# Performance work log

Hardware: AMD Instinct MI355X
Metric: run time of the kernel (lower is better)

The kernel has to match this reference:

```python
import jax, jax.numpy as jnp
import numpy as np

V, H, P, L, O = 47, 1024, 4, 3, 47
B, T = 256, 128


def setup_inputs() -> dict:
    key = jax.random.key(0)
    ks = jax.random.split(key, 10)
    s = 1.0 / np.sqrt(H)
    b_ih = jnp.zeros((L, 4 * H), jnp.float32).at[:, H:2 * H].set(1.0)  # forget-gate bias = 1
    return {
        "x": jax.random.randint(ks[0], (B, T), 0, V),
        "properties": jax.random.normal(ks[1], (B, P), jnp.float32),
        "emb": jax.random.normal(ks[2], (V, H), jnp.float32) * s,
        "W_dec": jax.random.normal(ks[3], (O, H), jnp.float32) * s,
        "b_dec": jnp.zeros((O,), jnp.float32),
        "W_ih0": jax.random.normal(ks[4], (4 * H, H + P), jnp.float32) * s,
        "W_ih_rest": jax.random.normal(ks[5], (L - 1, 4 * H, H), jnp.float32) * s,
        "W_hh": jax.random.normal(ks[6], (L, 4 * H, H), jnp.float32) * s,
        "b_ih": b_ih,
        "b_hh": jnp.zeros((L, 4 * H), jnp.float32),
    }


def _lstm_step(x_in, h, c, W_ih, W_hh, b_ih, b_hh):
    # x_in: [B, in_dim]; h, c: [B, H]; gate order i,f,g,o (PyTorch)
    gates = x_in @ W_ih.T + h @ W_hh.T + b_ih + b_hh  # [B, 4H]
    i, f, g, o = jnp.split(gates, 4, axis=-1)
    c_new = jax.nn.sigmoid(f) * c + jax.nn.sigmoid(i) * jnp.tanh(g)
    h_new = jax.nn.sigmoid(o) * jnp.tanh(c_new)
    return h_new, c_new


def reference(x, properties, emb, W_dec, b_dec, W_ih0, W_ih_rest, W_hh, b_ih, b_hh):
    bsz, max_length = x.shape
    h0 = jnp.zeros((L, bsz, H), emb.dtype)
    c0 = jnp.zeros((L, bsz, H), emb.dtype)
    inp0 = emb[jnp.zeros((bsz,), jnp.int32)]  # initial token id 0 -> [B, H]

    def step(carry, _):
        h, c, inp = carry
        x_in = jnp.concatenate([inp, properties], axis=-1)  # [B, H+P]
        hs, cs = [], []
        for l in range(L):
            W_ih_l = W_ih0 if l == 0 else W_ih_rest[l - 1]
            h_l, c_l = _lstm_step(x_in, h[l], c[l], W_ih_l, W_hh[l], b_ih[l], b_hh[l])
            hs.append(h_l); cs.append(c_l)
            x_in = h_l
        logits = x_in @ W_dec.T + b_dec  # [B, O]
        nxt = jnp.argmax(logits, axis=-1)  # greedy decode
        new_carry = (jnp.stack(hs), jnp.stack(cs), emb[nxt])
        return new_carry, logits

    (h, c, _), logits_seq = jax.lax.scan(step, (h0, c0, inp0), None, length=max_length)
    outputs = jnp.transpose(logits_seq, (1, 0, 2))  # [B, T, O]
    return outputs, h, c
```

## Files before the change

kernel.cpp:

```cpp
#include <hip/hip_runtime.h>
#include <hip/hip_bf16.h>
#include <cstdint>
#include <cstddef>


#define BB 256
#define TT 128
#define OO 47

typedef __attribute__((ext_vector_type(8))) _Float16 f16x8;
typedef __attribute__((ext_vector_type(4))) float f32x4;

#define CBUF_B   0u
#define HF32_B   3145728u
#define BCOMB_B  9437184u
#define EHI_B    9486336u
#define ELO_B    10027008u
#define HS_B     10567680u
#define W_B      16859136u
#define WS_NEEDED 118046720u

__device__ __forceinline__ float fsig(float x) {
  return 1.0f / (1.0f + exp2f(-1.4426950408889634f * x));
}
__device__ __forceinline__ float ftanhf(float x) {
  float e = exp2f(2.8853900817779268f * x);
  return 1.0f - 2.0f / (e + 1.0f);
}
__device__ __forceinline__ unsigned short f16b(_Float16 h) {
  union { _Float16 f; unsigned short u; } c; c.f = h; return c.u;
}
__device__ __forceinline__ void gld16(const void* g, void* l) {
  __builtin_amdgcn_global_load_lds(
      (const __attribute__((address_space(1))) unsigned int*)g,
      (__attribute__((address_space(3))) unsigned int*)l, 16, 0, 0);
}
__device__ __forceinline__ size_t slab_addr(int grp, int NCH, int k, int r) {
  return ((size_t)grp * NCH + (k >> 5)) * 512 + ((k >> 4) & 1) * 256 +
         ((k >> 3) & 1) * 128 + r * 8 + (k & 7);
}

__global__ void k_zero(float* p, int n) {
  int i = blockIdx.x * blockDim.x + threadIdx.x;
  int stride = gridDim.x * blockDim.x;
  for (; i < n; i += stride) p[i] = 0.0f;
}

__global__ void k_binit(float* bc, const float* __restrict__ bih,
                        const float* __restrict__ bhh) {
  int i = blockIdx.x * blockDim.x + threadIdx.x;
  if (i < 12288) bc[i] = bih[i] + bhh[i];
}

__global__ void k_prepw(const float* __restrict__ src, unsigned short* dhi,
                        unsigned short* dlo, int K, int NCH) {
  const int nrow = blockIdx.x;
  const int ngrp = nrow >> 4, rr = nrow & 15;
  const float* s = src + (size_t)nrow * K;
  for (int k = threadIdx.x; k < NCH * 32; k += blockDim.x) {
    float val = (k < K) ? s[k] : 0.0f;
    _Float16 h16 = (_Float16)val;
    _Float16 l16 = (_Float16)((val - (float)h16) * 2048.0f);
    size_t a = slab_addr(ngrp, NCH, k, rr);
    dhi[a] = f16b(h16);
    dlo[a] = f16b(l16);
  }
}

__global__ void k_einit(unsigned short* ehi, unsigned short* elo,
                        const float* __restrict__ emb,
                        const float* __restrict__ props) {
  const int b = blockIdx.x;
  for (int j = threadIdx.x; j < 1056; j += blockDim.x) {
    float val = (j < 1024) ? emb[j] : (j < 1028 ? props[b * 4 + (j - 1024)] : 0.0f);
    _Float16 h16 = (_Float16)val;
    _Float16 l16 = (_Float16)((val - (float)h16) * 2048.0f);
    size_t a = slab_addr(b >> 4, 33, j, b & 15);
    ehi[a] = f16b(h16);
    elo[a] = f16b(l16);
  }
}

__global__ __launch_bounds__(512, 2) void k_layer(
    const char* __restrict__ xhi, const char* __restrict__ xlo, int NCHX,
    const char* __restrict__ hhi, const char* __restrict__ hlo,
    const char* __restrict__ wxhi, const char* __restrict__ wxlo,
    const char* __restrict__ whhi, const char* __restrict__ whlo,
    const float* __restrict__ bcomb, float* __restrict__ cbuf,
    float* __restrict__ hdstf, unsigned short* __restrict__ hshi,
    unsigned short* __restrict__ hslo) {
  __shared__ char LBUF[65536];
  const int tid = threadIdx.x;
  const int lane = tid & 63, wid = tid >> 6;
  const int sw = ((blockIdx.x & 7) << 5) + (blockIdx.x >> 3);
  const int mt = sw & 3, nt = sw >> 2;
  const int m0 = mt << 6, h0c = nt << 4;
  const int nst = (NCHX > 32) ? NCHX : 32;

  const int sIsB = wid >> 2, sHalfW = (wid >> 1) & 1, sPrec = wid & 1;
  const int sNch = sHalfW ? 32 : NCHX;
  const char* sbase[4];
  {
    const char* t0;
    if (!sIsB) t0 = sHalfW ? (sPrec ? hlo : hhi) : (sPrec ? xlo : xhi);
    else       t0 = sHalfW ? (sPrec ? whlo : whhi) : (sPrec ? wxlo : wxhi);
#pragma unroll
    for (int i = 0; i < 4; ++i) {
      int grp = sIsB ? (i * 64 + nt) : (mt * 4 + i);
      sbase[i] = t0 + (size_t)grp * sNch * 1024 + (size_t)lane * 16;
    }
  }
  const int ldsoff0 = (sIsB << 14) + (sHalfW << 13) + (sPrec << 12);
  auto stage = [&](int s, int buf) {
    char* ldst = LBUF + buf * 32768 + ldsoff0;
    const size_t so = (size_t)s * 1024;
#pragma unroll
    for (int i = 0; i < 4; ++i) gld16(sbase[i] + so, ldst + i * 1024);
  };

  const int wHalf = wid >> 2, q = wid & 3;
  const int mb = (q >> 1) << 1, nbb = (q & 1) << 1;
  const int waveNst = wHalf ? 32 : NCHX;

  f32x4 accH[4], accL[4];
#pragma unroll
  for (int i = 0; i < 4; ++i) {
    accH[i] = f32x4{0.f, 0.f, 0.f, 0.f};
    accL[i] = f32x4{0.f, 0.f, 0.f, 0.f};
  }

  stage(0, 0);
  __syncthreads();

  for (int s = 0; s < nst; ++s) {
    const int cur = s & 1, nxt = cur ^ 1;
    if (s + 1 < sNch) stage(s + 1, nxt);

    if (s < waveNst) {
      const char* A0 = LBUF + cur * 32768 + (wHalf << 13);
      const char* B0 = LBUF + cur * 32768 + 16384 + (wHalf << 13);
      f16x8 ah[2], al[2], bh[2], bl[2];
#pragma unroll
      for (int r = 0; r < 2; ++r) {
        ah[r] = *(const f16x8*)(A0 + ((mb + r) << 10) + (lane << 4));
        al[r] = *(const f16x8*)(A0 + 4096 + ((mb + r) << 10) + (lane << 4));
      }
#pragma unroll
      for (int c = 0; c < 2; ++c) {
        bh[c] = *(const f16x8*)(B0 + ((nbb + c) << 10) + (lane << 4));
        bl[c] = *(const f16x8*)(B0 + 4096 + ((nbb + c) << 10) + (lane << 4));
      }
#pragma unroll
      for (int r = 0; r < 2; ++r)
#pragma unroll
        for (int c = 0; c < 2; ++c) {
          int ix = r * 2 + c;
          accH[ix] = __builtin_amdgcn_mfma_f32_16x16x32_f16(ah[r], bh[c], accH[ix], 0, 0, 0);
          accL[ix] = __builtin_amdgcn_mfma_f32_16x16x32_f16(al[r], bh[c], accL[ix], 0, 0, 0);
          accL[ix] = __builtin_amdgcn_mfma_f32_16x16x32_f16(ah[r], bl[c], accL[ix], 0, 0, 0);
        }
    }
    __syncthreads();
  }

  float* GH = (float*)LBUF;
  float* GL = GH + 64 * 68;
  const int mrow0 = ((q >> 1) << 5) + ((lane >> 4) << 2);
  const int ncol0 = ((q & 1) << 5) + (lane & 15);
  if (wHalf == 0) {
#pragma unroll
    for (int r = 0; r < 2; ++r)
#pragma unroll
      for (int c = 0; c < 2; ++c) {
        f32x4 aH = accH[r * 2 + c], aL = accL[r * 2 + c];
        int mr = mrow0 + r * 16, nc = ncol0 + c * 16;
#pragma unroll
        for (int i = 0; i < 4; ++i) {
          GH[(mr + i) * 68 + nc] = aH[i];
          GL[(mr + i) * 68 + nc] = aL[i];
        }
      }
  }
  __syncthreads();
  if (wHalf == 1) {
#pragma unroll
    for (int r = 0; r < 2; ++r)
#pragma unroll
      for (int c = 0; c < 2; ++c) {
        f32x4 aH = accH[r * 2 + c], aL = accL[r * 2 + c];
        int mr = mrow0 + r * 16, nc = ncol0 + c * 16;
#pragma unroll
        for (int i = 0; i < 4; ++i) {
          GH[(mr + i) * 68 + nc] += aH[i];
          GL[(mr + i) * 68 + nc] += aL[i];
        }
      }
  }
  __syncthreads();

  const float LSC = 1.0f / 2048.0f;
#pragma unroll
  for (int e = 0; e < 2; ++e) {
    int ci = tid * 2 + e;
    int bl_ = ci >> 4, hh = ci & 15;
    int b = m0 + bl_, hcol = h0c + hh;
    float xi = GH[bl_ * 68 + hh]      + GL[bl_ * 68 + hh]      * LSC + bcomb[hcol];
    float xf = GH[bl_ * 68 + 16 + hh] + GL[bl_ * 68 + 16 + hh] * LSC + bcomb[1024 + hcol];
    float xg = GH[bl_ * 68 + 32 + hh] + GL[bl_ * 68 + 32 + hh] * LSC + bcomb[2048 + hcol];
    float xo = GH[bl_ * 68 + 48 + hh] + GL[bl_ * 68 + 48 + hh] * LSC + bcomb[3072 + hcol];
    size_t cidx = (size_t)b * 1024 + hcol;
    float cn = fsig(xf) * cbuf[cidx] + fsig(xi) * ftanhf(xg);
    float hn = fsig(xo) * ftanhf(cn);
    cbuf[cidx] = cn;
    hdstf[cidx] = hn;
    _Float16 h16 = (_Float16)hn;
    _Float16 l16 = (_Float16)((hn - (float)h16) * 2048.0f);
    size_t sa = slab_addr(b >> 4, 32, hcol, b & 15);
    hshi[sa] = f16b(h16);
    hslo[sa] = f16b(l16);
  }
}

__global__ __launch_bounds__(256) void k_decode(
    const float* __restrict__ h2, const float* __restrict__ Wdec,
    const float* __restrict__ bdec, const float* __restrict__ emb,
    float* __restrict__ out, unsigned short* __restrict__ ehi,
    unsigned short* __restrict__ elo, int t) {
  __shared__ float P[4][64];
  __shared__ int tokS;
  const int b = blockIdx.x;
  const int w = threadIdx.x >> 6, lane = threadIdx.x & 63;
  const float* hrow = h2 + (size_t)b * 1024 + w * 256;
  float part = 0.f;
  if (lane < OO) {
    const float* wrow = Wdec + (size_t)lane * 1024 + w * 256;
    float p0 = 0.f, p1 = 0.f, p2 = 0.f, p3 = 0.f;
    for (int k = 0; k < 256; k += 16) {
      float4 w0 = *(const float4*)(wrow + k);      float4 h0v = *(const float4*)(hrow + k);
      float4 w1 = *(const float4*)(wrow + k + 4);  float4 h1v = *(const float4*)(hrow + k + 4);
      float4 w2 = *(const float4*)(wrow + k + 8);  float4 h2v = *(const float4*)(hrow + k + 8);
      float4 w3 = *(const float4*)(wrow + k + 12); float4 h3v = *(const float4*)(hrow + k + 12);
      p0 += w0.x * h0v.x + w0.y * h0v.y + w0.z * h0v.z + w0.w * h0v.w;
      p1 += w1.x * h1v.x + w1.y * h1v.y + w1.z * h1v.z + w1.w * h1v.w;
      p2 += w2.x * h2v.x + w2.y * h2v.y + w2.z * h2v.z + w2.w * h2v.w;
      p3 += w3.x * h3v.x + w3.y * h3v.y + w3.z * h3v.z + w3.w * h3v.w;
    }
    part = (p0 + p1) + (p2 + p3);
  }
  P[w][lane] = part;
  __syncthreads();
  if (w == 0) {
    float logit = -3.0e38f;
    if (lane < OO)
      logit = P[0][lane] + P[1][lane] + P[2][lane] + P[3][lane] + bdec[lane];
    float vv = logit;
    int idx = (lane < OO) ? lane : 1000;
#pragma unroll
    for (int m = 1; m < 64; m <<= 1) {
      float v2 = __shfl_xor(vv, m, 64);
      int i2 = __shfl_xor(idx, m, 64);
      if (v2 > vv || (v2 == vv && i2 < idx)) { vv = v2; idx = i2; }
    }
    if (lane < OO) out[(size_t)b * (TT * OO) + t * OO + lane] = logit;
    if (lane == 0) tokS = idx;
  }
  __syncthreads();
  if (t < TT - 1) {
    const float* erow = emb + (size_t)tokS * 1024;
    float4 ev = ((const float4*)erow)[threadIdx.x];
    float vals[4] = {ev.x, ev.y, ev.z, ev.w};
#pragma unroll
    for (int r = 0; r < 4; ++r) {
      int j = threadIdx.x * 4 + r;
      _Float16 h16 = (_Float16)vals[r];
      _Float16 l16 = (_Float16)((vals[r] - (float)h16) * 2048.0f);
      size_t a = slab_addr(b >> 4, 33, j, b & 15);
      ehi[a] = f16b(h16);
      elo[a] = f16b(l16);
    }
  }
}

__global__ void k_final(const float* __restrict__ hf, const float* __restrict__ cb,
                        float* __restrict__ out) {
  int i = blockIdx.x * blockDim.x + threadIdx.x;
  int stride = gridDim.x * blockDim.x;
  const int HBASE = BB * TT * OO;
  for (; i < 2 * 786432; i += stride) {
    if (i < 786432) {
      int l = i >> 18, r = i & 262143;
      out[HBASE + i] = hf[(size_t)(l * 2 + 0) * 262144 + r];
    } else {
      int j = i - 786432;
      out[HBASE + 786432 + j] = cb[j];
    }
  }
}

#define O_EBUF  0
#define O_HPB   270336
#define O_CBUF  1843200
#define O_BCOMB 2629632
#define O_WSN   2641920
#define O_HP(l, p) (O_HPB + ((l) * 2 + (p)) * 262144)

__global__ void k_initO(float* ws, const float* __restrict__ props,
                        const float* __restrict__ emb,
                        const float* __restrict__ bih,
                        const float* __restrict__ bhh) {
  int i = blockIdx.x * blockDim.x + threadIdx.x;
  if (i < 270336) {
    int b = i / 1056, j = i % 1056;
    float v = 0.0f;
    if (j < 1024) v = emb[j];
    else if (j < 1028) v = props[b * 4 + (j - 1024)];
    ws[O_EBUF + i] = v;
  } else if (i < 270336 + 12288) {
    int j = i - 270336;
    ws[O_BCOMB + j] = bih[j] + bhh[j];
  }
}

__global__ __launch_bounds__(512, 2) void k_layerO(
    const float* __restrict__ xsrc, int xs, int Kx, int nst0,
    const float* __restrict__ hsrc,
    const float* __restrict__ Wx, int wxs,
    const float* __restrict__ Wh,
    const float* __restrict__ bcomb, float* __restrict__ cbuf,
    float* __restrict__ hdst) {
  __shared__ char LBUF[65536];
  const int tid = threadIdx.x;
  const int lane = tid & 63, wid = tid >> 6;
  const int sw = ((blockIdx.x & 7) << 5) + (blockIdx.x >> 3);
  const int mt = sw & 3, nt = sw >> 2;
  const int m0 = mt << 6, h0c = nt << 4;
  const int nstMax = (nst0 > 32) ? nst0 : 32;
  const int tile = tid >> 7;
  const int tt = tid & 127;
  const int srow = tt >> 1;
  const int kseg = (tt & 1) << 4;
  const int isB = tile >> 1, sHalf = tile & 1;
  const int myNst = sHalf ? 32 : nst0;
  const float* grow;
  int KactB = 0x7fffffff;
  if (!isB) {
    grow = sHalf ? (hsrc + (size_t)(m0 + srow) * 1024)
                 : (xsrc + (size_t)(m0 + srow) * xs);
  } else {
    int nrow = ((srow >> 4) << 10) + h0c + (srow & 15);
    grow = sHalf ? (Wh + (size_t)nrow * 1024) : (Wx + (size_t)nrow * wxs);
    KactB = sHalf ? 1024 : Kx;
  }
  const int wbase = ((srow >> 4) << 10) + ((tt & 1) << 9) + ((srow & 15) << 4);
  const int ssec = (isB << 14) + (sHalf << 13);
  const int wHalf = wid >> 2, q = wid & 3;
  const int mb = (q >> 1) << 1, nbb = (q & 1) << 1;
  const int waveNst = wHalf ? 32 : nst0;
  const int secAr = (wHalf << 13);
  const int secBr = 16384 + (wHalf << 13);
  f32x4 accH[4], accL[4];
#pragma unroll
  for (int i = 0; i < 4; ++i) {
    accH[i] = f32x4{0.f, 0.f, 0.f, 0.f};
    accL[i] = f32x4{0.f, 0.f, 0.f, 0.f};
  }
  float4 v[4];
  auto load_regs = [&](int s) {
    const int kl = (s << 5) + kseg;
    const float4* p = (const float4*)(grow + kl);
#pragma unroll
    for (int qq = 0; qq < 4; ++qq) {
      int kk = kl + qq * 4;
      if (kk < KactB) v[qq] = p[qq];
      else v[qq] = float4{0.f, 0.f, 0.f, 0.f};
    }
  };
  auto cvt_write = [&](int buf) {
    char* base = LBUF + buf * 32768 + ssec + wbase;
#pragma unroll
    for (int g = 0; g < 2; ++g) {
      float fs[8] = {v[2*g].x, v[2*g].y, v[2*g].z, v[2*g].w,
                     v[2*g+1].x, v[2*g+1].y, v[2*g+1].z, v[2*g+1].w};
      f16x8 hvv, lvv;
#pragma unroll
      for (int j = 0; j < 8; ++j) {
        _Float16 h16 = (_Float16)fs[j];
        lvv[j] = (_Float16)((fs[j] - (float)h16) * 2048.0f);
        hvv[j] = h16;
      }
      *(f16x8*)(base + g * 256) = hvv;
      *(f16x8*)(base + g * 256 + 4096) = lvv;
    }
  };
  load_regs(0);
  cvt_write(0);
  __syncthreads();
  for (int s = 0; s < nstMax; ++s) {
    const int cur = s & 1, nxt = cur ^ 1;
    const bool doStage = (s + 1 < myNst);
    if (doStage) load_regs(s + 1);
    if (s < waveNst) {
      const char* A0 = LBUF + cur * 32768 + secAr;
      const char* B0 = LBUF + cur * 32768 + secBr;
      f16x8 ah[2], al[2], bh[2], bl[2];
#pragma unroll
      for (int r = 0; r < 2; ++r) {
        ah[r] = *(const f16x8*)(A0 + ((mb + r) << 10) + (lane << 4));
        al[r] = *(const f16x8*)(A0 + 4096 + ((mb + r) << 10) + (lane << 4));
      }
#pragma unroll
      for (int c = 0; c < 2; ++c) {
        bh[c] = *(const f16x8*)(B0 + ((nbb + c) << 10) + (lane << 4));
        bl[c] = *(const f16x8*)(B0 + 4096 + ((nbb + c) << 10) + (lane << 4));
      }
#pragma unroll
      for (int r = 0; r < 2; ++r)
#pragma unroll
        for (int c = 0; c < 2; ++c) {
          int ix = r * 2 + c;
          accH[ix] = __builtin_amdgcn_mfma_f32_16x16x32_f16(ah[r], bh[c], accH[ix], 0, 0, 0);
          accL[ix] = __builtin_amdgcn_mfma_f32_16x16x32_f16(al[r], bh[c], accL[ix], 0, 0, 0);
          accL[ix] = __builtin_amdgcn_mfma_f32_16x16x32_f16(ah[r], bl[c], accL[ix], 0, 0, 0);
        }
    }
    if (doStage) cvt_write(nxt);
    __syncthreads();
  }
  float* GH = (float*)LBUF;
  float* GL = GH + 64 * 68;
  const int mrow0 = ((q >> 1) << 5) + ((lane >> 4) << 2);
  const int ncol0 = ((q & 1) << 5) + (lane & 15);
  if (wHalf == 0) {
#pragma unroll
    for (int r = 0; r < 2; ++r)
#pragma unroll
      for (int c = 0; c < 2; ++c) {
        f32x4 aH = accH[r * 2 + c], aL = accL[r * 2 + c];
        int mr = mrow0 + r * 16, nc = ncol0 + c * 16;
#pragma unroll
        for (int i = 0; i < 4; ++i) { GH[(mr + i) * 68 + nc] = aH[i]; GL[(mr + i) * 68 + nc] = aL[i]; }
      }
  }
  __syncthreads();
  if (wHalf == 1) {
#pragma unroll
    for (int r = 0; r < 2; ++r)
#pragma unroll
      for (int c = 0; c < 2; ++c) {
        f32x4 aH = accH[r * 2 + c], aL = accL[r * 2 + c];
        int mr = mrow0 + r * 16, nc = ncol0 + c * 16;
#pragma unroll
        for (int i = 0; i < 4; ++i) { GH[(mr + i) * 68 + nc] += aH[i]; GL[(mr + i) * 68 + nc] += aL[i]; }
      }
  }
  __syncthreads();
  const float LSC = 1.0f / 2048.0f;
#pragma unroll
  for (int e = 0; e < 2; ++e) {
    int ci = tid * 2 + e;
    int bl_ = ci >> 4, hh = ci & 15;
    int b = m0 + bl_, hcol = h0c + hh;
    float xi = GH[bl_ * 68 + hh]      + GL[bl_ * 68 + hh]      * LSC + bcomb[hcol];
    float xf = GH[bl_ * 68 + 16 + hh] + GL[bl_ * 68 + 16 + hh] * LSC + bcomb[1024 + hcol];
    float xg = GH[bl_ * 68 + 32 + hh] + GL[bl_ * 68 + 32 + hh] * LSC + bcomb[2048 + hcol];
    float xo = GH[bl_ * 68 + 48 + hh] + GL[bl_ * 68 + 48 + hh] * LSC + bcomb[3072 + hcol];
    size_t cidx = (size_t)b * 1024 + hcol;
    float cn = fsig(xf) * cbuf[cidx] + fsig(xi) * ftanhf(xg);
    float hn = fsig(xo) * ftanhf(cn);
    cbuf[cidx] = cn;
    hdst[cidx] = hn;
  }
}

__global__ __launch_bounds__(64) void k_decodeO(
    const float* __restrict__ h2, const float* __restrict__ Wdec,
    const float* __restrict__ bdec, const float* __restrict__ emb,
    float* __restrict__ out, float* __restrict__ ebuf, int t) {
  const int b = blockIdx.x, lane = threadIdx.x;
  const float* hrow = h2 + (size_t)b * 1024;
  float logit = 0.f;
  if (lane < OO) {
    const float* wrow = Wdec + (size_t)lane * 1024;
    float p0 = 0.f, p1 = 0.f, p2 = 0.f, p3 = 0.f;
    for (int k = 0; k < 1024; k += 16) {
      float4 w0 = *(const float4*)(wrow + k);      float4 h0v = *(const float4*)(hrow + k);
      float4 w1 = *(const float4*)(wrow + k + 4);  float4 h1v = *(const float4*)(hrow + k + 4);
      float4 w2 = *(const float4*)(wrow + k + 8);  float4 h2v = *(const float4*)(hrow + k + 8);
      float4 w3 = *(const float4*)(wrow + k + 12); float4 h3v = *(const float4*)(hrow + k + 12);
      p0 += w0.x * h0v.x + w0.y * h0v.y + w0.z * h0v.z + w0.w * h0v.w;
      p1 += w1.x * h1v.x + w1.y * h1v.y + w1.z * h1v.z + w1.w * h1v.w;
      p2 += w2.x * h2v.x + w2.y * h2v.y + w2.z * h2v.z + w2.w * h2v.w;
      p3 += w3.x * h3v.x + w3.y * h3v.y + w3.z * h3v.z + w3.w * h3v.w;
    }
    logit = ((p0 + p1) + (p2 + p3)) + bdec[lane];
  }
  float vv = (lane < OO) ? logit : -3.0e38f;
  int idx = (lane < OO) ? lane : 1000;
#pragma unroll
  for (int m = 1; m < 64; m <<= 1) {
    float v2 = __shfl_xor(vv, m, 64);
    int i2 = __shfl_xor(idx, m, 64);
    if (v2 > vv || (v2 == vv && i2 < idx)) { vv = v2; idx = i2; }
  }
  if (lane < OO) out[(size_t)b * (TT * OO) + t * OO + lane] = logit;
  if (t < TT - 1) {
    const float* erow = emb + (size_t)idx * 1024;
#pragma unroll
    for (int i = 0; i < 16; ++i) {
      int h = i * 64 + lane;
      ebuf[(size_t)b * 1056 + h] = erow[h];
    }
  }
}

__global__ void k_finalO(const float* __restrict__ ws, float* __restrict__ out) {
  int i = blockIdx.x * blockDim.x + threadIdx.x;
  int stride = gridDim.x * blockDim.x;
  const int HBASE = BB * TT * OO;
  for (; i < 2 * 786432; i += stride) {
    if (i < 786432) {
      int l = i >> 18, r = i & 262143;
      out[HBASE + i] = ws[O_HP(l, 0) + r];
    } else {
      int j = i - 786432;
      out[HBASE + 786432 + j] = ws[O_CBUF + j];
    }
  }
}

extern "C" void kernel_launch(void* const* d_in, const int* in_sizes, int n_in,
                              void* d_out, int out_size, void* d_ws, size_t ws_size,
                              hipStream_t stream) {
  const float* props = (const float*)d_in[1];
  const float* emb   = (const float*)d_in[2];
  const float* Wdec  = (const float*)d_in[3];
  const float* bdec  = (const float*)d_in[4];
  const float* Wih0  = (const float*)d_in[5];
  const float* Wihr  = (const float*)d_in[6];
  const float* Whh   = (const float*)d_in[7];
  const float* bih   = (const float*)d_in[8];
  const float* bhh   = (const float*)d_in[9];
  float* out = (float*)d_out;

  if (ws_size >= (size_t)WS_NEEDED) {
    char* base = (char*)d_ws;
    float* cb = (float*)(base + CBUF_B);
    float* hf = (float*)(base + HF32_B);
    float* bc = (float*)(base + BCOMB_B);
    unsigned short* Ehi = (unsigned short*)(base + EHI_B);
    unsigned short* Elo = (unsigned short*)(base + ELO_B);
    auto HS = [&](int l, int p, int prec) {
      return (unsigned short*)(base + HS_B + (size_t)((l * 2 + p) * 2 + prec) * 524288u);
    };
    unsigned short* Wp[12];
    {
      size_t off = W_B;
      Wp[0] = (unsigned short*)(base + off); off += 8650752u;
      Wp[1] = (unsigned short*)(base + off); off += 8650752u;
      for (int i = 2; i < 12; ++i) { Wp[i] = (unsigned short*)(base + off); off += 8388608u; }
    }

    k_zero<<<2048, 256, 0, stream>>>((float*)base, 2359296);
    k_zero<<<2048, 256, 0, stream>>>((float*)(base + HS_B), 1572864);
    k_binit<<<48, 256, 0, stream>>>(bc, bih, bhh);
    k_einit<<<256, 256, 0, stream>>>(Ehi, Elo, emb, props);
    k_prepw<<<4096, 256, 0, stream>>>(Wih0, Wp[0], Wp[1], 1028, 33);
    k_prepw<<<4096, 256, 0, stream>>>(Whh,                          Wp[2], Wp[3], 1024, 32);
    k_prepw<<<4096, 256, 0, stream>>>(Wihr,                         Wp[4], Wp[5], 1024, 32);
    k_prepw<<<4096, 256, 0, stream>>>(Whh + (size_t)4096 * 1024,    Wp[6], Wp[7], 1024, 32);
    k_prepw<<<4096, 256, 0, stream>>>(Wihr + (size_t)4096 * 1024,   Wp[8], Wp[9], 1024, 32);
    k_prepw<<<4096, 256, 0, stream>>>(Whh + (size_t)2 * 4096 * 1024, Wp[10], Wp[11], 1024, 32);

    for (int t = 0; t < TT; ++t) {
      const int p = t & 1, pn = p ^ 1;
      k_layer<<<256, 512, 0, stream>>>(
          (const char*)Ehi, (const char*)Elo, 33,
          (const char*)HS(0, p, 0), (const char*)HS(0, p, 1),
          (const char*)Wp[0], (const char*)Wp[1],
          (const char*)Wp[2], (const char*)Wp[3],
          bc, cb, hf + (size_t)(0 * 2 + pn) * 262144,
          HS(0, pn, 0), HS(0, pn, 1));
      k_layer<<<256, 512, 0, stream>>>(
          (const char*)HS(0, pn, 0), (const char*)HS(0, pn, 1), 32,
          (const char*)HS(1, p, 0), (const char*)HS(1, p, 1),
          (const char*)Wp[4], (const char*)Wp[5],
          (const char*)Wp[6], (const char*)Wp[7],
          bc + 4096, cb + 262144, hf + (size_t)(1 * 2 + pn) * 262144,
          HS(1, pn, 0), HS(1, pn, 1));
      k_layer<<<256, 512, 0, stream>>>(
          (const char*)HS(1, pn, 0), (const char*)HS(1, pn, 1), 32,
          (const char*)HS(2, p, 0), (const char*)HS(2, p, 1),
          (const char*)Wp[8], (const char*)Wp[9],
          (const char*)Wp[10], (const char*)Wp[11],
          bc + 8192, cb + 524288, hf + (size_t)(2 * 2 + pn) * 262144,
          HS(2, pn, 0), HS(2, pn, 1));
      k_decode<<<256, 256, 0, stream>>>(hf + (size_t)(2 * 2 + pn) * 262144,
                                        Wdec, bdec, emb, out, Ehi, Elo, t);
    }
    k_final<<<2048, 256, 0, stream>>>(hf, cb, out);
  } else {
    float* ws = (float*)d_ws;
    float* E  = ws + O_EBUF;
    float* cb = ws + O_CBUF;
    float* bc = ws + O_BCOMB;
    k_zero<<<2048, 256, 0, stream>>>(ws, O_WSN);
    k_initO<<<1104, 256, 0, stream>>>(ws, props, emb, bih, bhh);
    for (int t = 0; t < TT; ++t) {
      const int p = t & 1;
      k_layerO<<<256, 512, 0, stream>>>(E, 1056, 1028, 33, ws + O_HP(0, p),
                                        Wih0, 1028, Whh, bc, cb, ws + O_HP(0, p ^ 1));
      k_layerO<<<256, 512, 0, stream>>>(ws + O_HP(0, p ^ 1), 1024, 1024, 32,
                                        ws + O_HP(1, p), Wihr, 1024,
                                        Whh + (size_t)4096 * 1024,
                                        bc + 4096, cb + 262144, ws + O_HP(1, p ^ 1));
      k_layerO<<<256, 512, 0, stream>>>(ws + O_HP(1, p ^ 1), 1024, 1024, 32,
                                        ws + O_HP(2, p),
                                        Wihr + (size_t)4096 * 1024, 1024,
                                        Whh + (size_t)2 * 4096 * 1024,
                                        bc + 8192, cb + 524288, ws + O_HP(2, p ^ 1));
      k_decodeO<<<256, 64, 0, stream>>>(ws + O_HP(2, p ^ 1), Wdec, bdec, emb, out, E, t);
    }
    k_finalO<<<2048, 256, 0, stream>>>(ws, out);
  }
}
```

Before: 11.20 ms.

## Split LSTM layer GEMM along K with atomic-counter reduction and 3-stage pipeline

The per-layer kernel changes tiling. Each block now covers all 256 batch rows for 16 hidden columns and one quarter of the K dimension (x-part or h-part), so each weight slab is loaded once per step rather than once per batch tile. Partial sums go to a global buffer, and the last block to finish, detected by an atomic counter, reduces them and applies the gate nonlinearities. The double-buffered LDS loop becomes a triple-buffered async-load pipeline with explicit waitcnt/barrier control and a larger LDS footprint (120 KB). The costs are a global round-trip for the partials, a serial tail in the finishing blocks, and lower occupancy.

```diff
diff --git a/kernel.cpp b/kernel.cpp
--- a/kernel.cpp
+++ b/kernel.cpp
@@ -18,7 +18,13 @@
 #define ELO_B    10027008u
 #define HS_B     10567680u
 #define W_B      16859136u
-#define WS_NEEDED 118046720u
+#define PART_B   118046720u
+#define CNT_B    134823936u
+#define WS_NEEDED 134824960u
+
+#define BARRIER() asm volatile("s_barrier" ::: "memory")
+#define WAITV(n)  asm volatile("s_waitcnt vmcnt(" #n ")" ::: "memory")
+#define WAITLGKM0() asm volatile("s_waitcnt lgkmcnt(0)" ::: "memory")
 
 __device__ __forceinline__ float fsig(float x) {
   return 1.0f / (1.0f + exp2f(-1.4426950408889634f * x));
@@ -47,9 +53,10 @@
 }
 
 __global__ void k_binit(float* bc, const float* __restrict__ bih,
-                        const float* __restrict__ bhh) {
+                        const float* __restrict__ bhh, unsigned* cnt) {
   int i = blockIdx.x * blockDim.x + threadIdx.x;
   if (i < 12288) bc[i] = bih[i] + bhh[i];
+  if (i < 64) cnt[i] = 0u;
 }
 
 __global__ void k_prepw(const float* __restrict__ src, unsigned short* dhi,
@@ -81,143 +88,182 @@
   }
 }
 
-__global__ __launch_bounds__(512, 2) void k_layer(
-    const char* __restrict__ xhi, const char* __restrict__ xlo, int NCHX,
-    const char* __restrict__ hhi, const char* __restrict__ hlo,
-    const char* __restrict__ wxhi, const char* __restrict__ wxlo,
-    const char* __restrict__ whhi, const char* __restrict__ whlo,
+__global__ __launch_bounds__(512, 2) void k_layer7(
+    const unsigned short* __restrict__ xhi, const unsigned short* __restrict__ xlo,
+    int NCHX,
+    const unsigned short* __restrict__ hhi, const unsigned short* __restrict__ hlo,
+    const unsigned short* __restrict__ wxhi, const unsigned short* __restrict__ wxlo,
+    const unsigned short* __restrict__ whhi, const unsigned short* __restrict__ whlo,
     const float* __restrict__ bcomb, float* __restrict__ cbuf,
     float* __restrict__ hdstf, unsigned short* __restrict__ hshi,
-    unsigned short* __restrict__ hslo) {
-  __shared__ char LBUF[65536];
+    unsigned short* __restrict__ hslo, float* __restrict__ part,
+    unsigned* __restrict__ cnt) {
+  __shared__ char LBUF[122880];
+  __shared__ int finFlag;
   const int tid = threadIdx.x;
   const int lane = tid & 63, wid = tid >> 6;
-  const int sw = ((blockIdx.x & 7) << 5) + (blockIdx.x >> 3);
-  const int mt = sw & 3, nt = sw >> 2;
-  const int m0 = mt << 6, h0c = nt << 4;
-  const int nst = (NCHX > 32) ? NCHX : 32;
-
-  const int sIsB = wid >> 2, sHalfW = (wid >> 1) & 1, sPrec = wid & 1;
-  const int sNch = sHalfW ? 32 : NCHX;
-  const char* sbase[4];
+  const int bid = blockIdx.x;
+  const int kq = (bid & 7) >> 1;
+  const int nt = ((bid & 1) << 5) | (bid >> 3);
+  const int h0c = nt << 4;
+
+  const unsigned short *Ahi, *Alo, *Whi, *Wlo;
+  int NCH, base, nst;
+  if (kq < 2) {
+    Ahi = xhi; Alo = xlo; Whi = wxhi; Wlo = wxlo;
+    NCH = NCHX; base = kq ? (NCHX - 16) : 0; nst = kq ? 16 : (NCHX - 16);
+  } else {
+    Ahi = hhi; Alo = hlo; Whi = whhi; Wlo = whlo;
+    NCH = 32; base = (kq - 2) << 4; nst = 16;
+  }
+
+  const char* sb[5];
+  int ldoff[5];
+#pragma unroll
+  for (int i = 0; i < 5; ++i) {
+    int j = wid * 5 + i;
+    const unsigned short* s_;
+    int grp;
+    if (j < 32) { grp = j >> 1; s_ = (j & 1) ? Alo : Ahi; }
+    else { int jj = j - 32; grp = (jj >> 1) * 64 + nt; s_ = (jj & 1) ? Wlo : Whi; }
+    sb[i] = (const char*)s_ + ((size_t)grp * NCH + base) * 1024 + (size_t)lane * 16;
+    ldoff[i] = j * 1024;
+  }
+  auto stage = [&](int s, int bufbase) {
+    const size_t so = (size_t)s * 1024;
+#pragma unroll
+    for (int i = 0; i < 5; ++i) gld16(sb[i] + so, LBUF + bufbase + ldoff[i]);
+  };
+
+  const int wm = wid & 3, wn = wid >> 2;
+  f32x4 aH[8], aL[8];
+#pragma unroll
+  for (int i = 0; i < 8; ++i) {
+    aH[i] = f32x4{0.f, 0.f, 0.f, 0.f};
+    aL[i] = f32x4{0.f, 0.f, 0.f, 0.f};
+  }
+
+  stage(0, 0);
+  stage(1, 40960);
+  stage(2, 81920);
+
+  int bufb = 0;
+  for (int s = 0; s < nst; ++s) {
+    if (s + 2 < nst)      { WAITV(10); }
+    else if (s + 1 < nst) { WAITV(5); }
+    else                  { WAITV(0); }
+    BARRIER();
+
+    {
+      const char* Bb = LBUF + bufb;
+      f16x8 a_h[4], a_l[4], w_h[2], w_l[2];
+#pragma unroll
+      for (int mf = 0; mf < 4; ++mf) {
+        int slab = ((wm << 2) + mf) << 1;
+        a_h[mf] = *(const f16x8*)(Bb + slab * 1024 + (lane << 4));
+        a_l[mf] = *(const f16x8*)(Bb + (slab + 1) * 1024 + (lane << 4));
+      }
+#pragma unroll
+      for (int nf = 0; nf < 2; ++nf) {
+        int slab = 32 + (((wn << 1) + nf) << 1);
+        w_h[nf] = *(const f16x8*)(Bb + slab * 1024 + (lane << 4));
+        w_l[nf] = *(const f16x8*)(Bb + (slab + 1) * 1024 + (lane << 4));
+      }
+#pragma unroll
+      for (int mf = 0; mf < 4; ++mf)
+#pragma unroll
+        for (int nf = 0; nf < 2; ++nf) {
+          int ix = mf * 2 + nf;
+          aH[ix] = __builtin_amdgcn_mfma_f32_16x16x32_f16(a_h[mf], w_h[nf], aH[ix], 0, 0, 0);
+          aL[ix] = __builtin_amdgcn_mfma_f32_16x16x32_f16(a_l[mf], w_h[nf], aL[ix], 0, 0, 0);
+          aL[ix] = __builtin_amdgcn_mfma_f32_16x16x32_f16(a_h[mf], w_l[nf], aL[ix], 0, 0, 0);
+        }
+    }
+
+    WAITLGKM0();
+    BARRIER();
+    if (s + 3 < nst) stage(s + 3, bufb);
+    bufb += 40960;
+    if (bufb == 122880) bufb = 0;
+  }
+
+  const float LSC = 1.0f / 2048.0f;
+  float* pslot = part + ((size_t)(nt * 4 + kq) * 256) * 64;
+#pragma unroll
+  for (int mf = 0; mf < 4; ++mf)
+#pragma unroll
+    for (int nf = 0; nf < 2; ++nf) {
+      int ix = mf * 2 + nf;
+#pragma unroll
+      for (int i = 0; i < 4; ++i) {
+        int m = (wm << 6) + (mf << 4) + ((lane >> 4) << 2) + i;
+        int n = (((wn << 1) + nf) << 4) + (lane & 15);
+        __hip_atomic_store(&pslot[(size_t)m * 64 + n], aH[ix][i] + aL[ix][i] * LSC,
+                           __ATOMIC_RELAXED, __HIP_MEMORY_SCOPE_AGENT);
+      }
+    }
+  __syncthreads();
+  if (tid == 0) {
+    unsigned old = __hip_atomic_fetch_add(&cnt[nt], 1u, __ATOMIC_ACQ_REL,
+                                          __HIP_MEMORY_SCOPE_AGENT);
+    finFlag = (old == 3u);
+  }
+  __syncthreads();
+  if (!finFlag) return;
+  if (tid == 0)
+    __hip_atomic_store(&cnt[nt], 0u, __ATOMIC_RELAXED, __HIP_MEMORY_SCOPE_AGENT);
+
+  float* G = (float*)LBUF;
   {
-    const char* t0;
-    if (!sIsB) t0 = sHalfW ? (sPrec ? hlo : hhi) : (sPrec ? xlo : xhi);
-    else       t0 = sHalfW ? (sPrec ? whlo : whhi) : (sPrec ? wxlo : wxhi);
-#pragma unroll
-    for (int i = 0; i < 4; ++i) {
-      int grp = sIsB ? (i * 64 + nt) : (mt * 4 + i);
-      sbase[i] = t0 + (size_t)grp * sNch * 1024 + (size_t)lane * 16;
-    }
-  }
-  const int ldsoff0 = (sIsB << 14) + (sHalfW << 13) + (sPrec << 12);
-  auto stage = [&](int s, int buf) {
-    char* ldst = LBUF + buf * 32768 + ldsoff0;
-    const size_t so = (size_t)s * 1024;
-#pragma unroll
-    for (int i = 0; i < 4; ++i) gld16(sbase[i] + so, ldst + i * 1024);
-  };
-
-  const int wHalf = wid >> 2, q = wid & 3;
-  const int mb = (q >> 1) << 1, nbb = (q & 1) << 1;
-  const int waveNst = wHalf ? 32 : NCHX;
-
-  f32x4 accH[4], accL[4];
-#pragma unroll
-  for (int i = 0; i < 4; ++i) {
-    accH[i] = f32x4{0.f, 0.f, 0.f, 0.f};
-    accL[i] = f32x4{0.f, 0.f, 0.f, 0.f};
-  }
-
-  stage(0, 0);
-  __syncthreads();
-
-  for (int s = 0; s < nst; ++s) {
-    const int cur = s & 1, nxt = cur ^ 1;
-    if (s + 1 < sNch) stage(s + 1, nxt);
-
-    if (s < waveNst) {
-      const char* A0 = LBUF + cur * 32768 + (wHalf << 13);
-      const char* B0 = LBUF + cur * 32768 + 16384 + (wHalf << 13);
-      f16x8 ah[2], al[2], bh[2], bl[2];
-#pragma unroll
-      for (int r = 0; r < 2; ++r) {
-        ah[r] = *(const f16x8*)(A0 + ((mb + r) << 10) + (lane << 4));
-        al[r] = *(const f16x8*)(A0 + 4096 + ((mb + r) << 10) + (lane << 4));
-      }
-#pragma unroll
-      for (int c = 0; c < 2; ++c) {
-        bh[c] = *(const f16x8*)(B0 + ((nbb + c) << 10) + (lane << 4));
-        bl[c] = *(const f16x8*)(B0 + 4096 + ((nbb + c) << 10) + (lane << 4));
-      }
-#pragma unroll
-      for (int r = 0; r < 2; ++r)
-#pragma unroll
-        for (int c = 0; c < 2; ++c) {
-          int ix = r * 2 + c;
-          accH[ix] = __builtin_amdgcn_mfma_f32_16x16x32_f16(ah[r], bh[c], accH[ix], 0, 0, 0);
-          accL[ix] = __builtin_amdgcn_mfma_f32_16x16x32_f16(al[r], bh[c], accL[ix], 0, 0, 0);
-          accL[ix] = __builtin_amdgcn_mfma_f32_16x16x32_f16(ah[r], bl[c], accL[ix], 0, 0, 0);
-        }
-    }
-    __syncthreads();
-  }
-
-  float* GH = (float*)LBUF;
-  float* GL = GH + 64 * 68;
-  const int mrow0 = ((q >> 1) << 5) + ((lane >> 4) << 2);
-  const int ncol0 = ((q & 1) << 5) + (lane & 15);
-  if (wHalf == 0) {
-#pragma unroll
-    for (int r = 0; r < 2; ++r)
-#pragma unroll
-      for (int c = 0; c < 2; ++c) {
-        f32x4 aH = accH[r * 2 + c], aL = accL[r * 2 + c];
-        int mr = mrow0 + r * 16, nc = ncol0 + c * 16;
-#pragma unroll
-        for (int i = 0; i < 4; ++i) {
-          GH[(mr + i) * 68 + nc] = aH[i];
-          GL[(mr + i) * 68 + nc] = aL[i];
-        }
-      }
-  }
-  __syncthreads();
-  if (wHalf == 1) {
-#pragma unroll
-    for (int r = 0; r < 2; ++r)
-#pragma unroll
-      for (int c = 0; c < 2; ++c) {
-        f32x4 aH = accH[r * 2 + c], aL = accL[r * 2 + c];
-        int mr = mrow0 + r * 16, nc = ncol0 + c * 16;
-#pragma unroll
-        for (int i = 0; i < 4; ++i) {
-          GH[(mr + i) * 68 + nc] += aH[i];
-          GL[(mr + i) * 68 + nc] += aL[i];
-        }
-      }
-  }
-  __syncthreads();
-
-  const float LSC = 1.0f / 2048.0f;
-#pragma unroll
-  for (int e = 0; e < 2; ++e) {
-    int ci = tid * 2 + e;
-    int bl_ = ci >> 4, hh = ci & 15;
-    int b = m0 + bl_, hcol = h0c + hh;
-    float xi = GH[bl_ * 68 + hh]      + GL[bl_ * 68 + hh]      * LSC + bcomb[hcol];
-    float xf = GH[bl_ * 68 + 16 + hh] + GL[bl_ * 68 + 16 + hh] * LSC + bcomb[1024 + hcol];
-    float xg = GH[bl_ * 68 + 32 + hh] + GL[bl_ * 68 + 32 + hh] * LSC + bcomb[2048 + hcol];
-    float xo = GH[bl_ * 68 + 48 + hh] + GL[bl_ * 68 + 48 + hh] * LSC + bcomb[3072 + hcol];
-    size_t cidx = (size_t)b * 1024 + hcol;
-    float cn = fsig(xf) * cbuf[cidx] + fsig(xi) * ftanhf(xg);
-    float hn = fsig(xo) * ftanhf(cn);
-    cbuf[cidx] = cn;
-    hdstf[cidx] = hn;
-    _Float16 h16 = (_Float16)hn;
-    _Float16 l16 = (_Float16)((hn - (float)h16) * 2048.0f);
-    size_t sa = slab_addr(b >> 4, 32, hcol, b & 15);
-    hshi[sa] = f16b(h16);
-    hslo[sa] = f16b(l16);
+    const int col = lane;
+    const float bias = bcomb[((col >> 4) << 10) + h0c + (col & 15)];
+    const float* p0 = part + ((size_t)(nt * 4 + 0) * 256) * 64;
+    const float* p1 = part + ((size_t)(nt * 4 + 1) * 256) * 64;
+    const float* p2 = part + ((size_t)(nt * 4 + 2) * 256) * 64;
+    const float* p3 = part + ((size_t)(nt * 4 + 3) * 256) * 64;
+#pragma unroll 4
+    for (int bi = 0; bi < 32; ++bi) {
+      int b = (wid << 5) + bi;
+      size_t o = (size_t)b * 64 + col;
+      float s0 = __hip_atomic_load(&p0[o], __ATOMIC_RELAXED, __HIP_MEMORY_SCOPE_AGENT);
+      float s1 = __hip_atomic_load(&p1[o], __ATOMIC_RELAXED, __HIP_MEMORY_SCOPE_AGENT);
+      float s2 = __hip_atomic_load(&p2[o], __ATOMIC_RELAXED, __HIP_MEMORY_SCOPE_AGENT);
+      float s3 = __hip_atomic_load(&p3[o], __ATOMIC_RELAXED, __HIP_MEMORY_SCOPE_AGENT);
+      G[b * 64 + col] = ((s0 + s1) + (s2 + s3)) + bias;
+    }
+  }
+  __syncthreads();
+
+  {
+    const int b = tid >> 1;
+    const int hh0 = (tid & 1) * 8;
+    float hn8[8];
+#pragma unroll
+    for (int k = 0; k < 8; ++k) {
+      int hh = hh0 + k;
+      float xi = G[b * 64 + hh];
+      float xf = G[b * 64 + 16 + hh];
+      float xg = G[b * 64 + 32 + hh];
+      float xo = G[b * 64 + 48 + hh];
+      int hcol = h0c + hh;
+      size_t cidx = (size_t)b * 1024 + hcol;
+      float cn = fsig(xf) * cbuf[cidx] + fsig(xi) * ftanhf(xg);
+      float hn = fsig(xo) * ftanhf(cn);
+      cbuf[cidx] = cn;
+      hdstf[cidx] = hn;
+      hn8[k] = hn;
+    }
+#pragma unroll
+    for (int k = 0; k < 8; k += 2) {
+      int hcol = h0c + hh0 + k;
+      size_t sa = slab_addr(b >> 4, 32, hcol, b & 15);
+      _Float16 h0 = (_Float16)hn8[k];
+      _Float16 h1 = (_Float16)hn8[k + 1];
+      _Float16 l0 = (_Float16)((hn8[k] - (float)h0) * 2048.0f);
+      _Float16 l1 = (_Float16)((hn8[k + 1] - (float)h1) * 2048.0f);
+      ((unsigned*)hshi)[sa >> 1] = (unsigned)f16b(h0) | ((unsigned)f16b(h1) << 16);
+      ((unsigned*)hslo)[sa >> 1] = (unsigned)f16b(l0) | ((unsigned)f16b(l1) << 16);
+    }
   }
 }
 
@@ -435,10 +481,10 @@
     for (int r = 0; r < 2; ++r)
 #pragma unroll
       for (int c = 0; c < 2; ++c) {
-        f32x4 aH = accH[r * 2 + c], aL = accL[r * 2 + c];
+        f32x4 aHh = accH[r * 2 + c], aLl = accL[r * 2 + c];
         int mr = mrow0 + r * 16, nc = ncol0 + c * 16;
 #pragma unroll
-        for (int i = 0; i < 4; ++i) { GH[(mr + i) * 68 + nc] = aH[i]; GL[(mr + i) * 68 + nc] = aL[i]; }
+        for (int i = 0; i < 4; ++i) { GH[(mr + i) * 68 + nc] = aHh[i]; GL[(mr + i) * 68 + nc] = aLl[i]; }
       }
   }
   __syncthreads();
@@ -447,10 +493,10 @@
     for (int r = 0; r < 2; ++r)
 #pragma unroll
       for (int c = 0; c < 2; ++c) {
-        f32x4 aH = accH[r * 2 + c], aL = accL[r * 2 + c];
+        f32x4 aHh = accH[r * 2 + c], aLl = accL[r * 2 + c];
         int mr = mrow0 + r * 16, nc = ncol0 + c * 16;
 #pragma unroll
-        for (int i = 0; i < 4; ++i) { GH[(mr + i) * 68 + nc] += aH[i]; GL[(mr + i) * 68 + nc] += aL[i]; }
+        for (int i = 0; i < 4; ++i) { GH[(mr + i) * 68 + nc] += aHh[i]; GL[(mr + i) * 68 + nc] += aLl[i]; }
       }
   }
   __syncthreads();
@@ -549,6 +595,8 @@
     float* bc = (float*)(base + BCOMB_B);
     unsigned short* Ehi = (unsigned short*)(base + EHI_B);
     unsigned short* Elo = (unsigned short*)(base + ELO_B);
+    float* part = (float*)(base + PART_B);
+    unsigned* cnt = (unsigned*)(base + CNT_B);
     auto HS = [&](int l, int p, int prec) {
       return (unsigned short*)(base + HS_B + (size_t)((l * 2 + p) * 2 + prec) * 524288u);
     };
@@ -562,38 +610,32 @@
 
     k_zero<<<2048, 256, 0, stream>>>((float*)base, 2359296);
     k_zero<<<2048, 256, 0, stream>>>((float*)(base + HS_B), 1572864);
-    k_binit<<<48, 256, 0, stream>>>(bc, bih, bhh);
+    k_binit<<<48, 256, 0, stream>>>(bc, bih, bhh, cnt);
     k_einit<<<256, 256, 0, stream>>>(Ehi, Elo, emb, props);
     k_prepw<<<4096, 256, 0, stream>>>(Wih0, Wp[0], Wp[1], 1028, 33);
-    k_prepw<<<4096, 256, 0, stream>>>(Whh,                          Wp[2], Wp[3], 1024, 32);
-    k_prepw<<<4096, 256, 0, stream>>>(Wihr,                         Wp[4], Wp[5], 1024, 32);
-    k_prepw<<<4096, 256, 0, stream>>>(Whh + (size_t)4096 * 1024,    Wp[6], Wp[7], 1024, 32);
-    k_prepw<<<4096, 256, 0, stream>>>(Wihr + (size_t)4096 * 1024,   Wp[8], Wp[9], 1024, 32);
+    k_prepw<<<4096, 256, 0, stream>>>(Whh,                           Wp[2], Wp[3], 1024, 32);
+    k_prepw<<<4096, 256, 0, stream>>>(Wihr,                          Wp[4], Wp[5], 1024, 32);
+    k_prepw<<<4096, 256, 0, stream>>>(Whh + (size_t)4096 * 1024,     Wp[6], Wp[7], 1024, 32);
+    k_prepw<<<4096, 256, 0, stream>>>(Wihr + (size_t)4096 * 1024,    Wp[8], Wp[9], 1024, 32);
     k_prepw<<<4096, 256, 0, stream>>>(Whh + (size_t)2 * 4096 * 1024, Wp[10], Wp[11], 1024, 32);
 
     for (int t = 0; t < TT; ++t) {
       const int p = t & 1, pn = p ^ 1;
-      k_layer<<<256, 512, 0, stream>>>(
-          (const char*)Ehi, (const char*)Elo, 33,
-          (const char*)HS(0, p, 0), (const char*)HS(0, p, 1),
-          (const char*)Wp[0], (const char*)Wp[1],
-          (const char*)Wp[2], (const char*)Wp[3],
+      k_layer7<<<256, 512, 0, stream>>>(
+          Ehi, Elo, 33, HS(0, p, 0), HS(0, p, 1),
+          Wp[0], Wp[1], Wp[2], Wp[3],
           bc, cb, hf + (size_t)(0 * 2 + pn) * 262144,
-          HS(0, pn, 0), HS(0, pn, 1));
-      k_layer<<<256, 512, 0, stream>>>(
-          (const char*)HS(0, pn, 0), (const char*)HS(0, pn, 1), 32,
-          (const char*)HS(1, p, 0), (const char*)HS(1, p, 1),
-          (const char*)Wp[4], (const char*)Wp[5],
-          (const char*)Wp[6], (const char*)Wp[7],
+          HS(0, pn, 0), HS(0, pn, 1), part, cnt);
+      k_layer7<<<256, 512, 0, stream>>>(
+          HS(0, pn, 0), HS(0, pn, 1), 32, HS(1, p, 0), HS(1, p, 1),
+          Wp[4], Wp[5], Wp[6], Wp[7],
           bc + 4096, cb + 262144, hf + (size_t)(1 * 2 + pn) * 262144,
-          HS(1, pn, 0), HS(1, pn, 1));
-      k_layer<<<256, 512, 0, stream>>>(
-          (const char*)HS(1, pn, 0), (const char*)HS(1, pn, 1), 32,
-          (const char*)HS(2, p, 0), (const char*)HS(2, p, 1),
-          (const char*)Wp[8], (const char*)Wp[9],
-          (const char*)Wp[10], (const char*)Wp[11],
+          HS(1, pn, 0), HS(1, pn, 1), part, cnt);
+      k_layer7<<<256, 512, 0, stream>>>(
+          HS(1, pn, 0), HS(1, pn, 1), 32, HS(2, p, 0), HS(2, p, 1),
+          Wp[8], Wp[9], Wp[10], Wp[11],
           bc + 8192, cb + 524288, hf + (size_t)(2 * 2 + pn) * 262144,
-          HS(2, pn, 0), HS(2, pn, 1));
+          HS(2, pn, 0), HS(2, pn, 1), part, cnt);
       k_decode<<<256, 256, 0, stream>>>(hf + (size_t)(2 * 2 + pn) * 262144,
                                         Wdec, bdec, emb, out, Ehi, Elo, t);
     }
```

Result: slower. 16.24 ms (+45.0%).
